# Kernel optimization log

Hardware: AMD Instinct MI355X
Metric: run time of the kernel (lower is better)

Reference implementation:

```python
import jax, jax.numpy as jnp
import numpy as np
from jax import lax

B, L, H = 16, 96, 128  # batch, encoder_input_size (seq/channels), hidden_size


def _same_pad(k):
    # torch Conv2d padding='same' (stride=1, dilation=1): left = (k-1)//2, extra on right
    t = k - 1
    return (t // 2, t - t // 2)


def setup_inputs() -> dict:
    key = jax.random.key(0)
    ks = jax.random.split(key, 10)
    return {
        "hidden": jax.random.normal(ks[0], (B, H), jnp.float32),
        "encoder_outputs": jax.random.normal(ks[1], (B, L, H), jnp.float32),
        "coverage": jax.random.uniform(ks[2], (B, L), jnp.float32),
        # attnConv: Conv2d(L, L, (H, H)) weight [out,in,kh,kw]
        "attn_conv_w": jax.random.normal(ks[3], (L, L, H, H), jnp.float32) * 0.02,
        "attn_conv_b": jax.random.normal(ks[4], (L,), jnp.float32) * 0.02,
        # cvgConv: Conv2d(L, L, (1, H))
        "cvg_conv_w": jax.random.normal(ks[5], (L, L, 1, H), jnp.float32) * 0.02,
        "cvg_conv_b": jax.random.normal(ks[6], (L,), jnp.float32) * 0.02,
        # decoderAttnLinear: Linear(H, H)
        "dec_w": jax.random.normal(ks[7], (H, H), jnp.float32) * 0.02,
        "dec_b": jax.random.normal(ks[8], (H,), jnp.float32) * 0.02,
        # v: Parameter [batch, hidden]
        "v": jax.random.normal(ks[9], (B, H), jnp.float32) * 0.1,
    }


def reference(hidden, encoder_outputs, coverage, attn_conv_w, attn_conv_b,
              cvg_conv_w, cvg_conv_b, dec_w, dec_b, v):
    dn = ("NCHW", "OIHW", "NCHW")
    # encoder features: conv over [B, L, 1, H] with (H, H) kernel, 'same' padding -> [B, L, 1, H]
    x = encoder_outputs[:, :, None, :]
    enc_f = lax.conv_general_dilated(
        x, attn_conv_w, (1, 1), [_same_pad(H), _same_pad(H)], dimension_numbers=dn
    ) + attn_conv_b[None, :, None, None]
    # decoder features: Linear(hidden) -> [B, 1, 1, H]
    dec_f = (hidden @ dec_w.T + dec_b)[:, None, None, :]
    # coverage features: conv over [B, L, 1, 1] with (1, H) kernel, 'same' -> [B, L, 1, 1]
    c = coverage[:, :, None, None]
    cvg_f = lax.conv_general_dilated(
        c, cvg_conv_w, (1, 1), [(0, 0), _same_pad(H)], dimension_numbers=dn
    ) + cvg_conv_b[None, :, None, None]
    # additive attention: tanh of summed features, project with v, softmax over L
    feats = jnp.tanh((enc_f + dec_f + cvg_f).reshape(B, L, H))
    scores = jnp.einsum("blh,bh->bl", feats, v)
    attn = jax.nn.softmax(scores, axis=1)
    new_coverage = coverage + attn
    context = jnp.einsum("bl,blh->bh", attn, encoder_outputs)
    return context, attn, new_coverage
```

## Files before the change

kernel.cpp:

```cpp
#include <hip/hip_runtime.h>
#include <hip/hip_bf16.h>
#include <hip/hip_fp16.h>
#include <math.h>

#define BB 16
#define LL 96
#define HH 128

typedef __attribute__((ext_vector_type(8))) short short8;
typedef __attribute__((ext_vector_type(4))) float f32x4;

#define WS_W    0
#define WS_E    589824
#define WS_DEC  983040
#define WS_CVG  985088
#define WS_SC   986624
#define WS_P    988160

__global__ __launch_bounds__(256) void prep_kernel(
        const float* __restrict__ hidden,
        const float* __restrict__ enc,
        const float* __restrict__ coverage,
        const float* __restrict__ attn_w,
        const float* __restrict__ cvg_w,
        const float* __restrict__ cvg_b,
        const float* __restrict__ dec_w,
        const float* __restrict__ dec_b,
        float* __restrict__ ws) {
    const int bid = blockIdx.x;
    const int tid = threadIdx.x;
    if (bid < 96) {
        const int i = bid;
        unsigned short* wout = (unsigned short*)(ws + WS_W);
        for (int idx = tid; idx < LL * HH; idx += 256) {
            const int o = idx >> 7, e = idx & 127;
            const int esrc = e ^ ((o & 7) << 3);
            float v = attn_w[(((size_t)o * LL + i) * HH + 63) * HH + esrc];
            __hip_bfloat16 h = __float2bfloat16(v);
            wout[(size_t)i * LL * HH + idx] = *(unsigned short*)&h;
        }
    } else if (bid < 112) {
        const int b = bid - 96;
        float* eout = ws + WS_E + (size_t)b * LL * 256;
        for (int idx = tid; idx < LL * 256; idx += 256) {
            const int i = idx >> 8, t = idx & 255;
            eout[idx] = (t >= 63 && t < 191) ? enc[((size_t)b * LL + i) * HH + (t - 63)] : 0.f;
        }
    } else {
        const int b = bid - 112;
        __shared__ float hid[HH];
        __shared__ float cov[LL];
        if (tid < HH) hid[tid] = hidden[b * HH + tid];
        if (tid < LL) cov[tid] = coverage[b * LL + tid];
        __syncthreads();
        if (tid < HH) {
            float acc = dec_b[tid];
            for (int k = 0; k < HH; ++k) acc += hid[k] * dec_w[tid * HH + k];
            ws[WS_DEC + b * HH + tid] = acc;
        } else if (tid < HH + LL) {
            const int t = tid - HH;
            float a2 = cvg_b[t];
            for (int i2 = 0; i2 < LL; ++i2)
                a2 += cov[i2] * cvg_w[((size_t)t * LL + i2) * HH + 63];
            ws[WS_CVG + b * LL + t] = a2;
        }
    }
}

__global__ __launch_bounds__(256) void mfma_kernel(float* __restrict__ ws) {
    const int kc = blockIdx.x;
    const int b  = blockIdx.y;
    const int tid  = threadIdx.x;
    const int lane = tid & 63;
    const int wg   = tid >> 6;
    const int lo   = lane & 15;
    const int hi   = lane >> 4;

    __shared__ __align__(16) short Abuf[LL * HH];
    __shared__ __align__(16) float Ebuf[256];

    f32x4 acc[6][2];
#pragma unroll
    for (int a = 0; a < 6; ++a)
#pragma unroll
        for (int c = 0; c < 2; ++c) acc[a][c] = f32x4{0.f, 0.f, 0.f, 0.f};

    const short* wsrc = (const short*)(ws + WS_W);
    const float* esrc = ws + WS_E + (size_t)b * LL * 256;

    for (int ii = 0; ii < 3; ++ii) {
        const int ig = kc * 3 + ii;
        __syncthreads();
        {
            const short8* s8 = (const short8*)(wsrc + (size_t)ig * LL * HH);
            short8* d8 = (short8*)Abuf;
#pragma unroll
            for (int t = 0; t < 6; ++t) d8[tid + t * 256] = s8[tid + t * 256];
            if (tid < 64)
                ((float4*)Ebuf)[tid] = ((const float4*)(esrc + ig * 256))[tid];
        }
        __syncthreads();

#pragma unroll
        for (int s = 0; s < 4; ++s) {
            short8 af[6];
#pragma unroll
            for (int ot = 0; ot < 6; ++ot) {
                const int o = ot * 16 + lo;
                const int idx8 = o * 16 + (((s << 2) + hi) ^ (o & 7));
                af[ot] = ((const short8*)Abuf)[idx8];
            }
#pragma unroll
            for (int wt = 0; wt < 2; ++wt) {
                const int t0 = s * 32 + hi * 8 + wg * 32 + wt * 16 + lo;
                union { short8 s8; __hip_bfloat16 h[8]; } bf;
#pragma unroll
                for (int j = 0; j < 8; ++j) bf.h[j] = __float2bfloat16(Ebuf[t0 + j]);
#pragma unroll
                for (int ot = 0; ot < 6; ++ot)
                    acc[ot][wt] = __builtin_amdgcn_mfma_f32_16x16x32_bf16(
                        af[ot], bf.s8, acc[ot][wt], 0, 0, 0);
            }
        }
    }

    __half* dst = (__half*)(ws + WS_P) + (size_t)(kc * BB + b) * LL * HH;
#pragma unroll
    for (int ot = 0; ot < 6; ++ot)
#pragma unroll
        for (int wt = 0; wt < 2; ++wt)
#pragma unroll
            for (int r = 0; r < 4; ++r) {
                const int o = ot * 16 + hi * 4 + r;
                const int w = wg * 32 + wt * 16 + lo;
                dst[o * HH + w] = __float2half(acc[ot][wt][r]);
            }
}

__global__ __launch_bounds__(128) void reduce_kernel(
        const float* __restrict__ attn_b,
        const float* __restrict__ vvec,
        float* __restrict__ ws) {
    const int o = blockIdx.x;
    const int b = blockIdx.y;
    const int h = threadIdx.x;
    const __half* p = (const __half*)(ws + WS_P) + ((size_t)b * LL + o) * HH + h;
    float sum = 0.f;
#pragma unroll
    for (int kc = 0; kc < 32; ++kc)
        sum += __half2float(p[(size_t)kc * BB * LL * HH]);
    float ef = sum + attn_b[o] + ws[WS_DEC + b * HH + h] + ws[WS_CVG + b * LL + o];
    float s = tanhf(ef) * vvec[b * HH + h];
#pragma unroll
    for (int off = 32; off > 0; off >>= 1) s += __shfl_down(s, off, 64);
    __shared__ float r2[2];
    if ((h & 63) == 0) r2[h >> 6] = s;
    __syncthreads();
    if (h == 0) ws[WS_SC + b * LL + o] = r2[0] + r2[1];
}

__global__ void finalize_kernel(const float* __restrict__ ws_scores,
                                const float* __restrict__ coverage,
                                const float* __restrict__ enc,
                                float* __restrict__ out) {
    int b = blockIdx.x;
    int t = threadIdx.x;
    __shared__ float sc[LL];
    __shared__ float at[LL];
    if (t < LL) sc[t] = ws_scores[b * LL + t];
    __syncthreads();

    float mx = -1e30f;
    for (int l = 0; l < LL; ++l) mx = fmaxf(mx, sc[l]);
    float sum = 0.f;
    for (int l = 0; l < LL; ++l) sum += expf(sc[l] - mx);

    if (t < LL) {
        float a = expf(sc[t] - mx) / sum;
        at[t] = a;
        out[BB * HH + b * LL + t] = a;
        out[BB * HH + BB * LL + b * LL + t] = coverage[b * LL + t] + a;
    }
    __syncthreads();

    float ctx = 0.f;
#pragma unroll 8
    for (int l = 0; l < LL; ++l) ctx += at[l] * enc[((size_t)b * LL + l) * HH + t];
    out[b * HH + t] = ctx;
}

extern "C" void kernel_launch(void* const* d_in, const int* in_sizes, int n_in,
                              void* d_out, int out_size, void* d_ws, size_t ws_size,
                              hipStream_t stream) {
    const float* hidden   = (const float*)d_in[0];
    const float* enc      = (const float*)d_in[1];
    const float* coverage = (const float*)d_in[2];
    const float* attn_w   = (const float*)d_in[3];
    const float* attn_b   = (const float*)d_in[4];
    const float* cvg_w    = (const float*)d_in[5];
    const float* cvg_b    = (const float*)d_in[6];
    const float* dec_w    = (const float*)d_in[7];
    const float* dec_b    = (const float*)d_in[8];
    const float* vvec     = (const float*)d_in[9];
    float* out = (float*)d_out;
    float* ws = (float*)d_ws;

    prep_kernel<<<128, 256, 0, stream>>>(hidden, enc, coverage, attn_w,
                                         cvg_w, cvg_b, dec_w, dec_b, ws);
    mfma_kernel<<<dim3(32, BB), 256, 0, stream>>>(ws);
    reduce_kernel<<<dim3(LL, BB), 128, 0, stream>>>(attn_b, vvec, ws);
    finalize_kernel<<<BB, HH, 0, stream>>>(ws + WS_SC, coverage, enc, out);
}
```

Baseline: 45.52 us.

## Fuse prep kernel into MFMA kernel, converting weights to bf16 on the fly

Removes the separate prep kernel. The MFMA kernel now reads the fp32 conv weight center row directly, converts it to bf16 with the swizzle while loading shared memory, and builds the zero-padded encoder row inline. Blocks with kc==0 also compute the decoder linear and coverage features. This saves one launch and the workspace round-trip. In exchange, each weight slice is re-read and re-converted by all 16 batch blocks, so global weight traffic is doubled (fp32 instead of bf16) and multiplied across batches.

```diff
diff --git a/kernel.cpp b/kernel.cpp
--- a/kernel.cpp
+++ b/kernel.cpp
@@ -10,14 +10,12 @@
 typedef __attribute__((ext_vector_type(8))) short short8;
 typedef __attribute__((ext_vector_type(4))) float f32x4;
 
-#define WS_W    0
-#define WS_E    589824
 #define WS_DEC  983040
 #define WS_CVG  985088
 #define WS_SC   986624
 #define WS_P    988160
 
-__global__ __launch_bounds__(256) void prep_kernel(
+__global__ __launch_bounds__(256) void mfma_kernel(
         const float* __restrict__ hidden,
         const float* __restrict__ enc,
         const float* __restrict__ coverage,
@@ -27,47 +25,6 @@
         const float* __restrict__ dec_w,
         const float* __restrict__ dec_b,
         float* __restrict__ ws) {
-    const int bid = blockIdx.x;
-    const int tid = threadIdx.x;
-    if (bid < 96) {
-        const int i = bid;
-        unsigned short* wout = (unsigned short*)(ws + WS_W);
-        for (int idx = tid; idx < LL * HH; idx += 256) {
-            const int o = idx >> 7, e = idx & 127;
-            const int esrc = e ^ ((o & 7) << 3);
-            float v = attn_w[(((size_t)o * LL + i) * HH + 63) * HH + esrc];
-            __hip_bfloat16 h = __float2bfloat16(v);
-            wout[(size_t)i * LL * HH + idx] = *(unsigned short*)&h;
-        }
-    } else if (bid < 112) {
-        const int b = bid - 96;
-        float* eout = ws + WS_E + (size_t)b * LL * 256;
-        for (int idx = tid; idx < LL * 256; idx += 256) {
-            const int i = idx >> 8, t = idx & 255;
-            eout[idx] = (t >= 63 && t < 191) ? enc[((size_t)b * LL + i) * HH + (t - 63)] : 0.f;
-        }
-    } else {
-        const int b = bid - 112;
-        __shared__ float hid[HH];
-        __shared__ float cov[LL];
-        if (tid < HH) hid[tid] = hidden[b * HH + tid];
-        if (tid < LL) cov[tid] = coverage[b * LL + tid];
-        __syncthreads();
-        if (tid < HH) {
-            float acc = dec_b[tid];
-            for (int k = 0; k < HH; ++k) acc += hid[k] * dec_w[tid * HH + k];
-            ws[WS_DEC + b * HH + tid] = acc;
-        } else if (tid < HH + LL) {
-            const int t = tid - HH;
-            float a2 = cvg_b[t];
-            for (int i2 = 0; i2 < LL; ++i2)
-                a2 += cov[i2] * cvg_w[((size_t)t * LL + i2) * HH + 63];
-            ws[WS_CVG + b * LL + t] = a2;
-        }
-    }
-}
-
-__global__ __launch_bounds__(256) void mfma_kernel(float* __restrict__ ws) {
     const int kc = blockIdx.x;
     const int b  = blockIdx.y;
     const int tid  = threadIdx.x;
@@ -85,19 +42,30 @@
 #pragma unroll
         for (int c = 0; c < 2; ++c) acc[a][c] = f32x4{0.f, 0.f, 0.f, 0.f};
 
-    const short* wsrc = (const short*)(ws + WS_W);
-    const float* esrc = ws + WS_E + (size_t)b * LL * 256;
-
     for (int ii = 0; ii < 3; ++ii) {
         const int ig = kc * 3 + ii;
         __syncthreads();
+#pragma unroll
+        for (int t = 0; t < 6; ++t) {
+            const int oct = tid + t * 256;
+            const int o = oct >> 4, a = oct & 15;
+            const int asrc = a ^ (o & 7);
+            const float* src = attn_w + (((size_t)o * LL + ig) * HH + 63) * HH + asrc * 8;
+            float4 f0 = *(const float4*)(src);
+            float4 f1 = *(const float4*)(src + 4);
+            union { unsigned short us[8]; short8 s8; } pk;
+            const float fv[8] = {f0.x, f0.y, f0.z, f0.w, f1.x, f1.y, f1.z, f1.w};
+#pragma unroll
+            for (int j = 0; j < 8; ++j) {
+                __hip_bfloat16 h = __float2bfloat16(fv[j]);
+                pk.us[j] = *(unsigned short*)&h;
+            }
+            ((short8*)Abuf)[oct] = pk.s8;
+        }
         {
-            const short8* s8 = (const short8*)(wsrc + (size_t)ig * LL * HH);
-            short8* d8 = (short8*)Abuf;
-#pragma unroll
-            for (int t = 0; t < 6; ++t) d8[tid + t * 256] = s8[tid + t * 256];
-            if (tid < 64)
-                ((float4*)Ebuf)[tid] = ((const float4*)(esrc + ig * 256))[tid];
+            float v = 0.f;
+            if (tid >= 63 && tid < 191) v = enc[((size_t)b * LL + ig) * HH + (tid - 63)];
+            Ebuf[tid] = v;
         }
         __syncthreads();
 
@@ -135,6 +103,21 @@
                 const int w = wg * 32 + wt * 16 + lo;
                 dst[o * HH + w] = __float2half(acc[ot][wt][r]);
             }
+
+    if (kc == 0) {
+        if (tid < HH) {
+            float acc2 = dec_b[tid];
+            for (int k = 0; k < HH; ++k)
+                acc2 += hidden[b * HH + k] * dec_w[tid * HH + k];
+            ws[WS_DEC + b * HH + tid] = acc2;
+        } else if (tid < HH + LL) {
+            const int t = tid - HH;
+            float a2 = cvg_b[t];
+            for (int i2 = 0; i2 < LL; ++i2)
+                a2 += coverage[b * LL + i2] * cvg_w[((size_t)t * LL + i2) * HH + 63];
+            ws[WS_CVG + b * LL + t] = a2;
+        }
+    }
 }
 
 __global__ __launch_bounds__(128) void reduce_kernel(
@@ -203,11 +186,10 @@
     const float* dec_b    = (const float*)d_in[8];
     const float* vvec     = (const float*)d_in[9];
     float* out = (float*)d_out;
-    float* ws = (float*)d_ws;
+    float* ws  = (float*)d_ws;
 
-    prep_kernel<<<128, 256, 0, stream>>>(hidden, enc, coverage, attn_w,
-                                         cvg_w, cvg_b, dec_w, dec_b, ws);
-    mfma_kernel<<<dim3(32, BB), 256, 0, stream>>>(ws);
+    mfma_kernel<<<dim3(32, BB), 256, 0, stream>>>(hidden, enc, coverage, attn_w,
+                                                  cvg_w, cvg_b, dec_w, dec_b, ws);
     reduce_kernel<<<dim3(LL, BB), 128, 0, stream>>>(attn_b, vvec, ws);
     finalize_kernel<<<BB, HH, 0, stream>>>(ws + WS_SC, coverage, enc, out);
 }
```

Result: slower. 49.79 us (+9.4%).

## Pre-pack encoder as bf16 pairs and fuse softmax finalize into reduce via last-block counter

Applied to the files above, without the earlier changes.

The prep kernel now stores the padded encoder rows as bf16 pairs in two parity-shifted copies, so the MFMA kernel loads B fragments with four 32-bit LDS reads instead of converting eight floats per fragment. The separate finalize kernel is folded into the reduce kernel: each block publishes its score and bumps a per-batch atomic counter, and the last block for a batch does the softmax, coverage and context. This removes one kernel launch and the per-fragment conversions. In exchange it adds atomics, a counter reset in prep, and a serial tail in one block per batch.

```diff
diff --git a/kernel.cpp b/kernel.cpp
--- a/kernel.cpp
+++ b/kernel.cpp
@@ -12,10 +12,11 @@
 
 #define WS_W    0
 #define WS_E    589824
-#define WS_DEC  983040
-#define WS_CVG  985088
-#define WS_SC   986624
-#define WS_P    988160
+#define WS_DEC  1007616
+#define WS_CVG  1009664
+#define WS_SC   1011200
+#define WS_CNT  1012736
+#define WS_P    1012752
 
 __global__ __launch_bounds__(256) void prep_kernel(
         const float* __restrict__ hidden,
@@ -41,13 +42,29 @@
         }
     } else if (bid < 112) {
         const int b = bid - 96;
-        float* eout = ws + WS_E + (size_t)b * LL * 256;
-        for (int idx = tid; idx < LL * 256; idx += 256) {
-            const int i = idx >> 8, t = idx & 255;
-            eout[idx] = (t >= 63 && t < 191) ? enc[((size_t)b * LL + i) * HH + (t - 63)] : 0.f;
+        unsigned int* eout = (unsigned int*)(ws + WS_E) + (size_t)b * LL * 272;
+        const float* esrc = enc + (size_t)b * LL * HH;
+        for (int idx = tid; idx < LL * 272; idx += 256) {
+            const int i = idx / 272, c = idx % 272;
+            int t0 = -1, t1 = -1;
+            if (c < 128) { t0 = 2 * c; t1 = 2 * c + 1; }
+            else if (c >= 129 && c < 257) { int q = c - 129; t0 = 2 * q + 1; t1 = 2 * q + 2; }
+            unsigned int lo16 = 0, hi16 = 0;
+            if (t0 >= 63 && t0 < 191) {
+                __hip_bfloat16 h = __float2bfloat16(esrc[i * HH + t0 - 63]);
+                lo16 = *(unsigned short*)&h;
+            }
+            if (t1 >= 63 && t1 < 191) {
+                __hip_bfloat16 h = __float2bfloat16(esrc[i * HH + t1 - 63]);
+                hi16 = *(unsigned short*)&h;
+            }
+            eout[idx] = lo16 | (hi16 << 16);
         }
     } else {
         const int b = bid - 112;
+        if (tid == 0)
+            __hip_atomic_store((int*)(ws + WS_CNT) + b, 0,
+                               __ATOMIC_RELAXED, __HIP_MEMORY_SCOPE_AGENT);
         __shared__ float hid[HH];
         __shared__ float cov[LL];
         if (tid < HH) hid[tid] = hidden[b * HH + tid];
@@ -77,7 +94,7 @@
     const int hi   = lane >> 4;
 
     __shared__ __align__(16) short Abuf[LL * HH];
-    __shared__ __align__(16) float Ebuf[256];
+    __shared__ __align__(16) unsigned int Ebuf[272];
 
     f32x4 acc[6][2];
 #pragma unroll
@@ -86,7 +103,7 @@
         for (int c = 0; c < 2; ++c) acc[a][c] = f32x4{0.f, 0.f, 0.f, 0.f};
 
     const short* wsrc = (const short*)(ws + WS_W);
-    const float* esrc = ws + WS_E + (size_t)b * LL * 256;
+    const unsigned int* esrc = (const unsigned int*)(ws + WS_E) + (size_t)b * LL * 272;
 
     for (int ii = 0; ii < 3; ++ii) {
         const int ig = kc * 3 + ii;
@@ -96,8 +113,8 @@
             short8* d8 = (short8*)Abuf;
 #pragma unroll
             for (int t = 0; t < 6; ++t) d8[tid + t * 256] = s8[tid + t * 256];
-            if (tid < 64)
-                ((float4*)Ebuf)[tid] = ((const float4*)(esrc + ig * 256))[tid];
+            if (tid < 68)
+                *(uint4*)&Ebuf[tid * 4] = *(const uint4*)(esrc + (size_t)ig * 272 + tid * 4);
         }
         __syncthreads();
 
@@ -113,9 +130,9 @@
 #pragma unroll
             for (int wt = 0; wt < 2; ++wt) {
                 const int t0 = s * 32 + hi * 8 + wg * 32 + wt * 16 + lo;
-                union { short8 s8; __hip_bfloat16 h[8]; } bf;
-#pragma unroll
-                for (int j = 0; j < 8; ++j) bf.h[j] = __float2bfloat16(Ebuf[t0 + j]);
+                const unsigned int* arr = Ebuf + ((lo & 1) ? 129 : 0) + (t0 >> 1);
+                union { uint4 u; short8 s8; } bf;
+                bf.u.x = arr[0]; bf.u.y = arr[1]; bf.u.z = arr[2]; bf.u.w = arr[3];
 #pragma unroll
                 for (int ot = 0; ot < 6; ++ot)
                     acc[ot][wt] = __builtin_amdgcn_mfma_f32_16x16x32_bf16(
@@ -137,14 +154,20 @@
             }
 }
 
-__global__ __launch_bounds__(128) void reduce_kernel(
+__global__ __launch_bounds__(128) void reduceF_kernel(
         const float* __restrict__ attn_b,
         const float* __restrict__ vvec,
-        float* __restrict__ ws) {
+        const float* __restrict__ coverage,
+        const float* __restrict__ enc,
+        float* __restrict__ ws,
+        float* __restrict__ out) {
     const int o = blockIdx.x;
     const int b = blockIdx.y;
     const int h = threadIdx.x;
     const __half* p = (const __half*)(ws + WS_P) + ((size_t)b * LL + o) * HH + h;
+    float* sc_ws = ws + WS_SC;
+    int* cnt = (int*)(ws + WS_CNT);
+
     float sum = 0.f;
 #pragma unroll
     for (int kc = 0; kc < 32; ++kc)
@@ -153,40 +176,42 @@
     float s = tanhf(ef) * vvec[b * HH + h];
 #pragma unroll
     for (int off = 32; off > 0; off >>= 1) s += __shfl_down(s, off, 64);
+
     __shared__ float r2[2];
+    __shared__ int isLast;
     if ((h & 63) == 0) r2[h >> 6] = s;
     __syncthreads();
-    if (h == 0) ws[WS_SC + b * LL + o] = r2[0] + r2[1];
-}
-
-__global__ void finalize_kernel(const float* __restrict__ ws_scores,
-                                const float* __restrict__ coverage,
-                                const float* __restrict__ enc,
-                                float* __restrict__ out) {
-    int b = blockIdx.x;
-    int t = threadIdx.x;
-    __shared__ float sc[LL];
-    __shared__ float at[LL];
-    if (t < LL) sc[t] = ws_scores[b * LL + t];
-    __syncthreads();
-
+    if (h == 0) {
+        float sc = r2[0] + r2[1];
+        __hip_atomic_store(&sc_ws[b * LL + o], sc,
+                           __ATOMIC_RELEASE, __HIP_MEMORY_SCOPE_AGENT);
+        int old = __hip_atomic_fetch_add(&cnt[b], 1,
+                                         __ATOMIC_ACQ_REL, __HIP_MEMORY_SCOPE_AGENT);
+        isLast = (old == LL - 1);
+    }
+    __syncthreads();
+    if (!isLast) return;
+
+    __shared__ float scl[LL], atl[LL];
+    if (h < LL)
+        scl[h] = __hip_atomic_load(&sc_ws[b * LL + h],
+                                   __ATOMIC_ACQUIRE, __HIP_MEMORY_SCOPE_AGENT);
+    __syncthreads();
     float mx = -1e30f;
-    for (int l = 0; l < LL; ++l) mx = fmaxf(mx, sc[l]);
-    float sum = 0.f;
-    for (int l = 0; l < LL; ++l) sum += expf(sc[l] - mx);
-
-    if (t < LL) {
-        float a = expf(sc[t] - mx) / sum;
-        at[t] = a;
-        out[BB * HH + b * LL + t] = a;
-        out[BB * HH + BB * LL + b * LL + t] = coverage[b * LL + t] + a;
-    }
-    __syncthreads();
-
-    float ctx = 0.f;
+    for (int l = 0; l < LL; ++l) mx = fmaxf(mx, scl[l]);
+    float den = 0.f;
+    for (int l = 0; l < LL; ++l) den += expf(scl[l] - mx);
+    if (h < LL) {
+        float a = expf(scl[h] - mx) / den;
+        atl[h] = a;
+        out[BB * HH + b * LL + h] = a;
+        out[BB * HH + BB * LL + b * LL + h] = coverage[b * LL + h] + a;
+    }
+    __syncthreads();
+    float c = 0.f;
 #pragma unroll 8
-    for (int l = 0; l < LL; ++l) ctx += at[l] * enc[((size_t)b * LL + l) * HH + t];
-    out[b * HH + t] = ctx;
+    for (int l = 0; l < LL; ++l) c += atl[l] * enc[((size_t)b * LL + l) * HH + h];
+    out[b * HH + h] = c;
 }
 
 extern "C" void kernel_launch(void* const* d_in, const int* in_sizes, int n_in,
@@ -203,11 +228,11 @@
     const float* dec_b    = (const float*)d_in[8];
     const float* vvec     = (const float*)d_in[9];
     float* out = (float*)d_out;
-    float* ws = (float*)d_ws;
+    float* ws  = (float*)d_ws;
 
     prep_kernel<<<128, 256, 0, stream>>>(hidden, enc, coverage, attn_w,
                                          cvg_w, cvg_b, dec_w, dec_b, ws);
     mfma_kernel<<<dim3(32, BB), 256, 0, stream>>>(ws);
-    reduce_kernel<<<dim3(LL, BB), 128, 0, stream>>>(attn_b, vvec, ws);
-    finalize_kernel<<<BB, HH, 0, stream>>>(ws + WS_SC, coverage, enc, out);
-}
+    reduceF_kernel<<<dim3(LL, BB), 128, 0, stream>>>(attn_b, vvec, coverage,
+                                                     enc, ws, out);
+}
```

Result: slower. 114.1 us (+150.7%).

## Double-buffer weight and encoder tiles in the MFMA kernel with register prefetch

Applied to the files above, without the earlier changes.

The MFMA kernel now loads the next weight slice and encoder row from global memory into registers while the MFMAs run on the current LDS buffer. The staged data is then written into a second LDS buffer. This hides global load latency behind compute and removes one barrier per iteration. In exchange, LDS use roughly doubles and register pressure rises, which could lower occupancy, and each block only runs three iterations, so there is little to overlap.

```diff
diff --git a/kernel.cpp b/kernel.cpp
--- a/kernel.cpp
+++ b/kernel.cpp
@@ -76,8 +76,8 @@
     const int lo   = lane & 15;
     const int hi   = lane >> 4;
 
-    __shared__ __align__(16) short Abuf[LL * HH];
-    __shared__ __align__(16) float Ebuf[256];
+    __shared__ __align__(16) short Abuf[2][LL * HH];
+    __shared__ __align__(16) float Ebuf[2][256];
 
     f32x4 acc[6][2];
 #pragma unroll
@@ -88,19 +88,22 @@
     const short* wsrc = (const short*)(ws + WS_W);
     const float* esrc = ws + WS_E + (size_t)b * LL * 256;
 
-    for (int ii = 0; ii < 3; ++ii) {
-        const int ig = kc * 3 + ii;
-        __syncthreads();
-        {
-            const short8* s8 = (const short8*)(wsrc + (size_t)ig * LL * HH);
-            short8* d8 = (short8*)Abuf;
-#pragma unroll
-            for (int t = 0; t < 6; ++t) d8[tid + t * 256] = s8[tid + t * 256];
-            if (tid < 64)
-                ((float4*)Ebuf)[tid] = ((const float4*)(esrc + ig * 256))[tid];
-        }
-        __syncthreads();
-
+    short8 sA[6];
+    float4 sE;
+
+    auto gload = [&](int r) {
+        const short8* s8 = (const short8*)(wsrc + (size_t)(kc * 3 + r) * LL * HH);
+#pragma unroll
+        for (int t = 0; t < 6; ++t) sA[t] = s8[tid + t * 256];
+        if (tid < 64) sE = ((const float4*)(esrc + (kc * 3 + r) * 256))[tid];
+    };
+    auto lwrite = [&](int buf) {
+        short8* d8 = (short8*)Abuf[buf];
+#pragma unroll
+        for (int t = 0; t < 6; ++t) d8[tid + t * 256] = sA[t];
+        if (tid < 64) ((float4*)Ebuf[buf])[tid] = sE;
+    };
+    auto compute = [&](int buf) {
 #pragma unroll
         for (int s = 0; s < 4; ++s) {
             short8 af[6];
@@ -108,21 +111,33 @@
             for (int ot = 0; ot < 6; ++ot) {
                 const int o = ot * 16 + lo;
                 const int idx8 = o * 16 + (((s << 2) + hi) ^ (o & 7));
-                af[ot] = ((const short8*)Abuf)[idx8];
+                af[ot] = ((const short8*)Abuf[buf])[idx8];
             }
 #pragma unroll
             for (int wt = 0; wt < 2; ++wt) {
                 const int t0 = s * 32 + hi * 8 + wg * 32 + wt * 16 + lo;
                 union { short8 s8; __hip_bfloat16 h[8]; } bf;
 #pragma unroll
-                for (int j = 0; j < 8; ++j) bf.h[j] = __float2bfloat16(Ebuf[t0 + j]);
+                for (int j = 0; j < 8; ++j) bf.h[j] = __float2bfloat16(Ebuf[buf][t0 + j]);
 #pragma unroll
                 for (int ot = 0; ot < 6; ++ot)
                     acc[ot][wt] = __builtin_amdgcn_mfma_f32_16x16x32_bf16(
                         af[ot], bf.s8, acc[ot][wt], 0, 0, 0);
             }
         }
-    }
+    };
+
+    gload(0); lwrite(0);
+    __syncthreads();
+    gload(1);
+    compute(0);
+    lwrite(1);
+    __syncthreads();
+    gload(2);
+    compute(1);
+    lwrite(0);
+    __syncthreads();
+    compute(0);
 
     __half* dst = (__half*)(ws + WS_P) + (size_t)(kc * BB + b) * LL * HH;
 #pragma unroll
```

New measurement: 42.17 us. 1.08x faster.
